# Kernel optimization log

Hardware: AMD Instinct MI355X
Metric: run time of the kernel (lower is better)

## Reference

```python
import jax, jax.numpy as jnp
import numpy as np

B, N, E = 64, 20000, 160000
F_TEXT, HID, OUT = 300, 1024, 1664
NEG_SLOPE = 0.2


def setup_inputs() -> dict:
    key = jax.random.key(0)
    ks = jax.random.split(key, 9)
    img_feat = jax.random.normal(ks[0], (B, OUT), dtype=jnp.float32)
    node_features = jax.random.normal(ks[1], (N, F_TEXT), dtype=jnp.float32)
    edge_src = jax.random.randint(ks[2], (E,), 0, N, dtype=jnp.int32)
    edge_dst = jax.random.randint(ks[3], (E,), 0, N, dtype=jnp.int32)
    edge_weight = jax.random.uniform(ks[4], (E,), dtype=jnp.float32)
    W1 = jax.random.normal(ks[5], (F_TEXT, HID), dtype=jnp.float32) / np.sqrt(F_TEXT)
    b1 = jax.random.normal(ks[6], (HID,), dtype=jnp.float32) * 0.01
    W2 = jax.random.normal(ks[7], (HID, OUT), dtype=jnp.float32) / np.sqrt(HID)
    b2 = jax.random.normal(ks[8], (OUT,), dtype=jnp.float32) * 0.01
    return {"img_feat": img_feat, "node_features": node_features,
            "edge_src": edge_src, "edge_dst": edge_dst, "edge_weight": edge_weight,
            "W1": W1, "b1": b1, "W2": W2, "b2": b2}


def _gcn_norm(edge_src, edge_dst, edge_weight, num_nodes):
    # PyG gcn_norm with add_self_loops=False: symmetric degree normalization
    deg = jax.ops.segment_sum(edge_weight, edge_dst, num_segments=num_nodes)
    dinv = jnp.where(deg > 0, jax.lax.rsqrt(deg), 0.0)
    return dinv[edge_src] * edge_weight * dinv[edge_dst]


def _gcn_conv(x, edge_src, edge_dst, norm, W, b):
    # GCNConv: linear transform, then normalized gather -> scatter-add, then bias
    h = x @ W  # [N, out]
    msgs = h[edge_src] * norm[:, None]  # [E, out] gather + scale
    agg = jax.ops.segment_sum(msgs, edge_dst, num_segments=x.shape[0])
    return agg + b


def reference(img_feat, node_features, edge_src, edge_dst, edge_weight, W1, b1, W2, b2):
    num_nodes = node_features.shape[0]
    norm = _gcn_norm(edge_src, edge_dst, edge_weight, num_nodes)
    x = _gcn_conv(node_features, edge_src, edge_dst, norm, W1, b1)
    x = jnp.where(x >= 0, x, NEG_SLOPE * x)  # leaky_relu(0.2)
    x = _gcn_conv(x, edge_src, edge_dst, norm, W2, b2)
    return img_feat @ x.T  # [B, N]
```

## Files before the change

kernel.cpp:

```cpp
#include <hip/hip_runtime.h>
#include <hip/hip_bf16.h>

#define NNODES 20000
#define NEDGES 160000
#define BQ     64
#define FTEXT  300
#define KPAD1  320
#define HIDDIM 1024
#define OUTDIM 1664

typedef __attribute__((ext_vector_type(8))) short short8;
typedef __attribute__((ext_vector_type(4))) float floatx4;

__device__ inline unsigned short f2bf(float f) {
    union { float f; unsigned int u; } v; v.f = f;
    unsigned int r = v.u + 0x7FFF + ((v.u >> 16) & 1);
    return (unsigned short)(r >> 16);
}
__device__ inline float bf2f(unsigned short h) {
    union { unsigned int u; float f; } v; v.u = ((unsigned int)h) << 16;
    return v.f;
}

__global__ void degcnt_kernel(const int* __restrict__ dst, const float* __restrict__ w,
                              float* __restrict__ deg, int* __restrict__ cnt, int E) {
    int e = blockIdx.x * blockDim.x + threadIdx.x;
    if (e < E) {
        int d = dst[e];
        atomicAdd(&deg[d], w[e]);
        atomicAdd(&cnt[d], 1);
    }
}

__global__ __launch_bounds__(1024) void scan_kernel(const int* __restrict__ cnt,
                                                    int* __restrict__ row_start, int N) {
    __shared__ int partial[1024];
    const int CH = 20;
    int t = threadIdx.x;
    int begin = t * CH;
    int nloc = N - begin; if (nloc > CH) nloc = CH; if (nloc < 0) nloc = 0;
    int vals[CH];
    int s = 0;
    if (nloc == CH) {
        #pragma unroll
        for (int i = 0; i < CH / 4; i++) {
            int4 v = ((const int4*)(cnt + begin))[i];
            vals[i*4+0] = v.x; vals[i*4+1] = v.y; vals[i*4+2] = v.z; vals[i*4+3] = v.w;
            s += v.x + v.y + v.z + v.w;
        }
    } else {
        for (int i = 0; i < nloc; i++) { vals[i] = cnt[begin + i]; s += vals[i]; }
    }
    partial[t] = s;
    __syncthreads();
    for (int off = 1; off < 1024; off <<= 1) {
        int v = (t >= off) ? partial[t - off] : 0;
        __syncthreads();
        partial[t] += v;
        __syncthreads();
    }
    int run = (t == 0) ? 0 : partial[t - 1];
    for (int i = 0; i < nloc; i++) { row_start[begin + i] = run; run += vals[i]; }
    if (t == 1023) row_start[N] = partial[1023];
}

__global__ void fill_kernel(const int* __restrict__ dst, const int* __restrict__ src,
                            const float* __restrict__ w, const float* __restrict__ deg,
                            const int* __restrict__ row_start, int* __restrict__ cursor,
                            int* __restrict__ src_s, float* __restrict__ wnrm_s, int E) {
    int e = blockIdx.x * blockDim.x + threadIdx.x;
    if (e < E) {
        int d = dst[e], s = src[e];
        float dd = deg[d], ds = deg[s];
        float nv = (ds > 0.f ? rsqrtf(ds) : 0.f) * w[e] * (dd > 0.f ? rsqrtf(dd) : 0.f);
        int pos = row_start[d] + atomicAdd(&cursor[d], 1);
        src_s[pos] = s;
        wnrm_s[pos] = nv;
    }
}

__global__ __launch_bounds__(256) void aggnf_kernel(const unsigned short* __restrict__ nfb,
        const int* __restrict__ row_start, const int* __restrict__ src_s,
        const float* __restrict__ wnrm_s, unsigned short* __restrict__ out) {
    int wave = threadIdx.x >> 6, lane = threadIdx.x & 63;
    int d = blockIdx.x * 4 + wave;
    int s0 = row_start[d], s1 = row_start[d + 1];
    float4 acc  = make_float4(0.f, 0.f, 0.f, 0.f);
    float4 acc2 = make_float4(0.f, 0.f, 0.f, 0.f);
    for (int base = s0; base < s1; base += 64) {
        int m = s1 - base; if (m > 64) m = 64;
        int   src_l = (lane < m) ? src_s[base + lane]  : 0;
        float w_l   = (lane < m) ? wnrm_s[base + lane] : 0.f;
        int sj = __shfl(src_l, 0);
        float wj = __shfl(w_l, 0);
        const ushort4* row = (const ushort4*)(nfb + (long)sj * FTEXT);
        ushort4 hv  = row[lane];
        ushort4 hv2 = make_ushort4(0, 0, 0, 0);
        if (lane < 11) hv2 = row[64 + lane];
        for (int j = 0; j < m; j++) {
            ushort4 nv  = make_ushort4(0, 0, 0, 0);
            ushort4 nv2 = make_ushort4(0, 0, 0, 0);
            float wn = 0.f;
            if (j + 1 < m) {
                int sn = __shfl(src_l, j + 1);
                wn = __shfl(w_l, j + 1);
                const ushort4* nrow = (const ushort4*)(nfb + (long)sn * FTEXT);
                nv = nrow[lane];
                if (lane < 11) nv2 = nrow[64 + lane];
            }
            acc.x  += bf2f(hv.x)  * wj; acc.y  += bf2f(hv.y)  * wj;
            acc.z  += bf2f(hv.z)  * wj; acc.w  += bf2f(hv.w)  * wj;
            acc2.x += bf2f(hv2.x) * wj; acc2.y += bf2f(hv2.y) * wj;
            acc2.z += bf2f(hv2.z) * wj; acc2.w += bf2f(hv2.w) * wj;
            hv = nv; hv2 = nv2; wj = wn;
        }
    }
    unsigned short* orow = out + (long)d * KPAD1;
    ushort4 o;
    o.x = f2bf(acc.x); o.y = f2bf(acc.y); o.z = f2bf(acc.z); o.w = f2bf(acc.w);
    ((ushort4*)orow)[lane] = o;
    if (lane < 16) {
        ushort4 o2 = make_ushort4(0, 0, 0, 0);
        if (lane < 11) {
            o2.x = f2bf(acc2.x); o2.y = f2bf(acc2.y);
            o2.z = f2bf(acc2.z); o2.w = f2bf(acc2.w);
        }
        ((ushort4*)orow)[64 + lane] = o2;
    }
}

#define W1N  (HIDDIM * KPAD1)
#define N1F4 (HIDDIM * OUTDIM / 4)
#define N2F4 (BQ * OUTDIM / 4)
#define N3F4 (NNODES * FTEXT / 4)
__global__ void cvt_all_kernel(const float* __restrict__ W1, unsigned short* __restrict__ W1ch,
                               const float* __restrict__ W2, unsigned short* __restrict__ W2b,
                               const float* __restrict__ img, unsigned short* __restrict__ imgb,
                               const float* __restrict__ nf, unsigned short* __restrict__ nfb) {
    int i = blockIdx.x * 256 + threadIdx.x;
    if (i < W1N) {
        int c   = i >> 12;
        int w   = i & 4095;
        int lqg = w >> 10;
        int row = (w >> 3) & 127;
        int j   = i & 7;
        int nt = c / 10, s = c - nt * 10;
        int n = nt * 128 + row;
        int k = s * 32 + lqg * 8 + j;
        float v = (k < FTEXT) ? W1[(long)k * HIDDIM + n] : 0.f;
        W1ch[i] = f2bf(v);
        return;
    }
    i -= W1N;
    const float* in; unsigned short* outp; int j;
    if (i < N1F4)                    { in = W2;  outp = W2b;  j = i; }
    else if (i < N1F4 + N2F4)        { in = img; outp = imgb; j = i - N1F4; }
    else if (i < N1F4 + N2F4 + N3F4) { in = nf;  outp = nfb;  j = i - N1F4 - N2F4; }
    else return;
    float4 v = ((const float4*)in)[j];
    ushort4 o;
    o.x = f2bf(v.x); o.y = f2bf(v.y); o.z = f2bf(v.z); o.w = f2bf(v.w);
    ((ushort4*)outp)[j] = o;
}

__global__ __launch_bounds__(256) void ztcvec_kernel(const float* __restrict__ Ztf,
        unsigned short* __restrict__ Zt, const float* __restrict__ img,
        const float* __restrict__ b2, float* __restrict__ cvec) {
    if (blockIdx.x < (BQ * HIDDIM) / 256) {
        int i = blockIdx.x * 256 + threadIdx.x;
        Zt[i] = f2bf(Ztf[i]);
    } else {
        int b = blockIdx.x - (BQ * HIDDIM) / 256;
        int l = threadIdx.x;
        float v = 0.f;
        for (int f = l; f < OUTDIM; f += 256) v += img[(long)b * OUTDIM + f] * b2[f];
        __shared__ float red[256];
        red[l] = v;
        __syncthreads();
        if (l < 64) {
            v = red[l] + red[l + 64] + red[l + 128] + red[l + 192];
            for (int off = 32; off > 0; off >>= 1) v += __shfl_down(v, off);
            if (l == 0) cvec[b] = v;
        }
    }
}

template<int EPI, int OUT_BF16, int ATOMIC, int NT>
__global__ __launch_bounds__(256) void mfma_gemm(
        const unsigned short* __restrict__ A, const unsigned short* __restrict__ B,
        const float* __restrict__ bias, void* __restrict__ Cv,
        int M, int N, int K, int ldc) {
    constexpr int CT = NT / 16;
    __shared__ unsigned short As[128][40];
    __shared__ unsigned short Bs[NT][40];
    int t = threadIdx.x;
    int m0 = blockIdx.y * 128;
    int n0 = blockIdx.x * NT;
    int klen = K / gridDim.z;
    int kbeg = blockIdx.z * klen;
    int wave = t >> 6, lane = t & 63;
    int lm = lane & 15, lq = lane >> 4;
    floatx4 acc[2][CT] = {};
    for (int k0 = kbeg; k0 < kbeg + klen; k0 += 32) {
        #pragma unroll
        for (int p = 0; p < 2; p++) {
            int idx = p * 256 + t;
            int r = idx >> 2, c8 = (idx & 3) * 8;
            uint4 v = make_uint4(0, 0, 0, 0);
            int gm = m0 + r;
            if (gm < M) v = *(const uint4*)(A + (long)gm * K + k0 + c8);
            *(uint4*)&As[r][c8] = v;
        }
        #pragma unroll
        for (int p = 0; p < NT / 64; p++) {
            int idx = p * 256 + t;
            int r = idx >> 2, c8 = (idx & 3) * 8;
            uint4 v = *(const uint4*)(B + (long)(n0 + r) * K + k0 + c8);
            *(uint4*)&Bs[r][c8] = v;
        }
        __syncthreads();
        short8 a[2], b[CT];
        #pragma unroll
        for (int rt = 0; rt < 2; rt++)
            a[rt] = *(const short8*)&As[wave * 32 + rt * 16 + lm][lq * 8];
        #pragma unroll
        for (int ct = 0; ct < CT; ct++)
            b[ct] = *(const short8*)&Bs[ct * 16 + lm][lq * 8];
        #pragma unroll
        for (int rt = 0; rt < 2; rt++)
            #pragma unroll
            for (int ct = 0; ct < CT; ct++)
                acc[rt][ct] = __builtin_amdgcn_mfma_f32_16x16x32_bf16(
                    a[rt], b[ct], acc[rt][ct], 0, 0, 0);
        __syncthreads();
    }
    #pragma unroll
    for (int rt = 0; rt < 2; rt++) {
        #pragma unroll
        for (int r = 0; r < 4; r++) {
            int gm = m0 + wave * 32 + rt * 16 + lq * 4 + r;
            if (gm >= M) continue;
            #pragma unroll
            for (int ct = 0; ct < CT; ct++) {
                int gn = n0 + ct * 16 + lm;
                float v = acc[rt][ct][r];
                if (EPI) { v += bias[gn]; v = v >= 0.f ? v : 0.2f * v; }
                if (OUT_BF16)      ((unsigned short*)Cv)[(long)gm * ldc + gn] = f2bf(v);
                else if (ATOMIC)   atomicAdd((float*)Cv + (long)gm * ldc + gn, v);
                else               ((float*)Cv)[(long)gm * ldc + gn] = v;
            }
        }
    }
}

__global__ __launch_bounds__(128, 2) void xy_gemm(
        const unsigned short* __restrict__ aggNF, const unsigned short* __restrict__ W1ch,
        const float* __restrict__ b1, const unsigned short* __restrict__ Zt,
        float* __restrict__ Y, int M) {
    __shared__ unsigned short xs[32][136];
    float (*ys)[68] = (float (*)[68])xs;
    int t = threadIdx.x;
    int wn = t >> 6, lane = t & 63;
    int lm = lane & 15, lq = lane >> 4;
    int m0 = blockIdx.x * 32;

    short8 afr[2][10];
    #pragma unroll
    for (int rt = 0; rt < 2; rt++) {
        const unsigned short* ap = aggNF + (long)(m0 + rt * 16 + lm) * KPAD1 + lq * 8;
        #pragma unroll
        for (int kk = 0; kk < 10; kk++)
            afr[rt][kk] = *(const short8*)(ap + kk * 32);
    }
    short8 bcur[4], bnxt[4];
    {
        const unsigned short* bp = W1ch + lq * 1024 + (wn * 64 + lm) * 8;
        #pragma unroll
        for (int ct = 0; ct < 4; ct++) bcur[ct] = *(const short8*)(bp + ct * 128);
    }
    floatx4 yacc[2][4] = {};
    for (int nt = 0; nt < 8; nt++) {
        floatx4 acc[2][4] = {};
        #pragma unroll
        for (int s = 0; s < 10; s++) {
            int c = nt * 10 + s + 1;
            const unsigned short* bp = W1ch + (long)c * 4096 + lq * 1024
                                            + (wn * 64 + lm) * 8;
            #pragma unroll
            for (int ct = 0; ct < 4; ct++) bnxt[ct] = *(const short8*)(bp + ct * 128);
            #pragma unroll
            for (int rt = 0; rt < 2; rt++)
                #pragma unroll
                for (int ct = 0; ct < 4; ct++)
                    acc[rt][ct] = __builtin_amdgcn_mfma_f32_16x16x32_bf16(
                        afr[rt][s], bcur[ct], acc[rt][ct], 0, 0, 0);
            #pragma unroll
            for (int ct = 0; ct < 4; ct++) bcur[ct] = bnxt[ct];
        }
        #pragma unroll
        for (int ct = 0; ct < 4; ct++) {
            int col = wn * 64 + ct * 16 + lm;
            float bv = b1[nt * 128 + col];
            #pragma unroll
            for (int rt = 0; rt < 2; rt++)
                #pragma unroll
                for (int r = 0; r < 4; r++) {
                    float v = acc[rt][ct][r] + bv;
                    v = v >= 0.f ? v : 0.2f * v;
                    xs[rt * 16 + lq * 4 + r][col] = f2bf(v);
                }
        }
        __syncthreads();
        #pragma unroll
        for (int kk2 = 0; kk2 < 2; kk2++) {
            #pragma unroll
            for (int rt = 0; rt < 2; rt++) {
                short8 a = *(const short8*)&xs[rt * 16 + lm][wn * 64 + kk2 * 32 + lq * 8];
                #pragma unroll
                for (int bt = 0; bt < 4; bt++) {
                    short8 b = *(const short8*)(Zt + (long)(bt * 16 + lm) * HIDDIM
                                                    + nt * 128 + wn * 64 + kk2 * 32 + lq * 8);
                    yacc[rt][bt] = __builtin_amdgcn_mfma_f32_16x16x32_bf16(
                        a, b, yacc[rt][bt], 0, 0, 0);
                }
            }
        }
        __syncthreads();
    }
    if (wn == 1) {
        #pragma unroll
        for (int rt = 0; rt < 2; rt++)
            #pragma unroll
            for (int bt = 0; bt < 4; bt++)
                #pragma unroll
                for (int r = 0; r < 4; r++)
                    ys[rt * 16 + lq * 4 + r][bt * 16 + lm] = yacc[rt][bt][r];
    }
    __syncthreads();
    if (wn == 0) {
        #pragma unroll
        for (int rt = 0; rt < 2; rt++)
            #pragma unroll
            for (int bt = 0; bt < 4; bt++)
                #pragma unroll
                for (int r = 0; r < 4; r++) {
                    int row = rt * 16 + lq * 4 + r;
                    Y[(long)(m0 + row) * 64 + bt * 16 + lm]
                        = yacc[rt][bt][r] + ys[row][bt * 16 + lm];
                }
    }
}

__global__ __launch_bounds__(256) void outagg_kernel(const float* __restrict__ Y,
        const int* __restrict__ row_start, const int* __restrict__ src_s,
        const float* __restrict__ wnrm_s, const float* __restrict__ c,
        float* __restrict__ out, int N) {
    __shared__ float tile[4][68];
    int d0 = blockIdx.x * 4;
    int t = threadIdx.x;
    int wave = t >> 6, lane = t & 63;
    int d = d0 + wave;
    int s0 = row_start[d], s1 = row_start[d + 1];
    float acc = 0.f;
    for (int base = s0; base < s1; base += 64) {
        int m = s1 - base; if (m > 64) m = 64;
        int   src_l = (lane < m) ? src_s[base + lane]  : 0;
        float w_l   = (lane < m) ? wnrm_s[base + lane] : 0.f;
        int sj = __shfl(src_l, 0);
        float wj = __shfl(w_l, 0);
        float yv = Y[(long)sj * 64 + lane];
        for (int j = 0; j < m; j++) {
            float yn = 0.f, wn = 0.f;
            if (j + 1 < m) {
                int sn = __shfl(src_l, j + 1);
                wn = __shfl(w_l, j + 1);
                yn = Y[(long)sn * 64 + lane];
            }
            acc += wj * yv;
            yv = yn; wj = wn;
        }
    }
    tile[wave][lane] = acc + c[lane];
    __syncthreads();
    int b = t >> 2, j = t & 3;
    out[(long)b * N + d0 + j] = tile[j][b];
}

extern "C" void kernel_launch(void* const* d_in, const int* in_sizes, int n_in,
                              void* d_out, int out_size, void* d_ws, size_t ws_size,
                              hipStream_t stream) {
    const float* img_feat      = (const float*)d_in[0];
    const float* node_features = (const float*)d_in[1];
    const int*   edge_src      = (const int*)d_in[2];
    const int*   edge_dst      = (const int*)d_in[3];
    const float* edge_weight   = (const float*)d_in[4];
    const float* W1            = (const float*)d_in[5];
    const float* b1            = (const float*)d_in[6];
    const float* W2            = (const float*)d_in[7];
    const float* b2            = (const float*)d_in[8];
    float* out = (float*)d_out;

    const int N = NNODES, E = NEDGES;

    char* ws = (char*)d_ws;
    size_t off = 0;
    auto alloc = [&](size_t bytes) -> void* {
        void* p = ws + off;
        off = (off + bytes + 255) & ~(size_t)255;
        return p;
    };
    float*          deg       = (float*)alloc((size_t)N * 4);
    int*            cnt       = (int*)alloc((size_t)N * 4);
    int*            cursor    = (int*)alloc((size_t)N * 4);
    float*          Ztf       = (float*)alloc((size_t)BQ * HIDDIM * 4);
    size_t zero_bytes = off;
    float*          Y         = (float*)alloc((size_t)N * BQ * 4);
    int*            row_start = (int*)alloc((size_t)(N + 1) * 4);
    int*            src_s     = (int*)alloc((size_t)E * 4);
    float*          wnrm_s    = (float*)alloc((size_t)E * 4);
    unsigned short* aggNF     = (unsigned short*)alloc((size_t)N * KPAD1 * 2);
    unsigned short* W1ch      = (unsigned short*)alloc(((size_t)HIDDIM * KPAD1 + 4096) * 2);
    unsigned short* W2b       = (unsigned short*)alloc((size_t)HIDDIM * OUTDIM * 2);
    unsigned short* imgb      = (unsigned short*)alloc((size_t)BQ * OUTDIM * 2);
    unsigned short* nfb       = (unsigned short*)alloc((size_t)N * FTEXT * 2);
    unsigned short* Zt        = (unsigned short*)alloc((size_t)BQ * HIDDIM * 2);
    float*          cvec      = (float*)alloc((size_t)BQ * 4);

    hipMemsetAsync(ws, 0, zero_bytes, stream);

    int eb = (E + 255) / 256;
    degcnt_kernel<<<eb, 256, 0, stream>>>(edge_dst, edge_weight, deg, cnt, E);
    scan_kernel<<<1, 1024, 0, stream>>>(cnt, row_start, N);
    fill_kernel<<<eb, 256, 0, stream>>>(edge_dst, edge_src, edge_weight, deg, row_start,
                                        cursor, src_s, wnrm_s, E);

    cvt_all_kernel<<<(W1N + (N1F4 + N2F4 + N3F4) + 255) / 256, 256, 0, stream>>>(
        W1, W1ch, W2, W2b, img_feat, imgb, node_features, nfb);

    mfma_gemm<0, 0, 1, 64><<<dim3(HIDDIM / 64, 1, 13), 256, 0, stream>>>(
        imgb, W2b, nullptr, Ztf, BQ, HIDDIM, OUTDIM, HIDDIM);
    ztcvec_kernel<<<(BQ * HIDDIM) / 256 + BQ, 256, 0, stream>>>(Ztf, Zt, img_feat, b2, cvec);

    aggnf_kernel<<<N / 4, 256, 0, stream>>>(nfb, row_start, src_s, wnrm_s, aggNF);

    xy_gemm<<<dim3(NNODES / 32), 128, 0, stream>>>(aggNF, W1ch, b1, Zt, Y, N);

    outagg_kernel<<<N / 4, 256, 0, stream>>>(Y, row_start, src_s, wnrm_s, cvec, out, N);
}
```

Before: 245.8 us.

## Stage W1 panels in LDS via async global_load_lds and split hidden dim across 4 waves

The fused hidden-layer/Y GEMM now loads each 64-column panel of the bf16 W1 into shared memory with direct global-to-LDS loads, instead of every wave streaming W1 fragments from global memory into registers. The block grows to 4 waves, each owning 16 hidden columns per panel and 16 of the 64 output columns of Y, so the final cross-wave reduction through shared memory goes away. W1 is re-laid out in the conversion kernel to match the panel order. The goal is to cut redundant global/L2 traffic for W1 and improve MFMA issue. The cost is a 40KB LDS buffer with extra barriers per panel, and the next panel's load may not fully overlap with compute.

```diff
diff --git a/kernel.cpp b/kernel.cpp
--- a/kernel.cpp
+++ b/kernel.cpp
@@ -20,6 +20,12 @@
 __device__ inline float bf2f(unsigned short h) {
     union { unsigned int u; float f; } v; v.u = ((unsigned int)h) << 16;
     return v.f;
+}
+
+__device__ inline void gload16(const unsigned short* g, unsigned short* l) {
+    __builtin_amdgcn_global_load_lds(
+        (const __attribute__((address_space(1))) unsigned int*)g,
+        (__attribute__((address_space(3))) unsigned int*)l, 16, 0, 0);
 }
 
 __global__ void degcnt_kernel(const int* __restrict__ dst, const float* __restrict__ w,
@@ -139,14 +145,14 @@
                                const float* __restrict__ nf, unsigned short* __restrict__ nfb) {
     int i = blockIdx.x * 256 + threadIdx.x;
     if (i < W1N) {
-        int c   = i >> 12;
-        int w   = i & 4095;
-        int lqg = w >> 10;
-        int row = (w >> 3) & 127;
-        int j   = i & 7;
-        int nt = c / 10, s = c - nt * 10;
-        int n = nt * 128 + row;
-        int k = s * 32 + lqg * 8 + j;
+        int p   = i / 20480;
+        int w   = i - p * 20480;
+        int s   = w >> 11;
+        int lq  = (w >> 9) & 3;
+        int col = (w >> 3) & 63;
+        int j   = w & 7;
+        int n = p * 64 + col;
+        int k = s * 32 + lq * 8 + j;
         float v = (k < FTEXT) ? W1[(long)k * HIDDIM + n] : 0.f;
         W1ch[i] = f2bf(v);
         return;
@@ -253,12 +259,12 @@
     }
 }
 
-__global__ __launch_bounds__(128, 2) void xy_gemm(
+__global__ __launch_bounds__(256, 3) void xy_gemm(
         const unsigned short* __restrict__ aggNF, const unsigned short* __restrict__ W1ch,
         const float* __restrict__ b1, const unsigned short* __restrict__ Zt,
         float* __restrict__ Y, int M) {
-    __shared__ unsigned short xs[32][136];
-    float (*ys)[68] = (float (*)[68])xs;
+    __shared__ unsigned short Bsh[20480];
+    __shared__ unsigned short xs[32][76];
     int t = threadIdx.x;
     int wn = t >> 6, lane = t & 63;
     int lm = lane & 15, lq = lane >> 4;
@@ -272,83 +278,57 @@
         for (int kk = 0; kk < 10; kk++)
             afr[rt][kk] = *(const short8*)(ap + kk * 32);
     }
-    short8 bcur[4], bnxt[4];
     {
-        const unsigned short* bp = W1ch + lq * 1024 + (wn * 64 + lm) * 8;
-        #pragma unroll
-        for (int ct = 0; ct < 4; ct++) bcur[ct] = *(const short8*)(bp + ct * 128);
-    }
-    floatx4 yacc[2][4] = {};
-    for (int nt = 0; nt < 8; nt++) {
-        floatx4 acc[2][4] = {};
+        const unsigned short* src = W1ch + t * 8;
+        #pragma unroll
+        for (int r = 0; r < 10; r++)
+            gload16(src + r * 2048, &Bsh[t * 8 + r * 2048]);
+    }
+    floatx4 yacc[2] = {};
+    for (int p = 0; p < 16; p++) {
+        __syncthreads();
+        floatx4 acc[2] = {};
         #pragma unroll
         for (int s = 0; s < 10; s++) {
-            int c = nt * 10 + s + 1;
-            const unsigned short* bp = W1ch + (long)c * 4096 + lq * 1024
-                                            + (wn * 64 + lm) * 8;
-            #pragma unroll
-            for (int ct = 0; ct < 4; ct++) bnxt[ct] = *(const short8*)(bp + ct * 128);
-            #pragma unroll
-            for (int rt = 0; rt < 2; rt++)
-                #pragma unroll
-                for (int ct = 0; ct < 4; ct++)
-                    acc[rt][ct] = __builtin_amdgcn_mfma_f32_16x16x32_bf16(
-                        afr[rt][s], bcur[ct], acc[rt][ct], 0, 0, 0);
-            #pragma unroll
-            for (int ct = 0; ct < 4; ct++) bcur[ct] = bnxt[ct];
-        }
-        #pragma unroll
-        for (int ct = 0; ct < 4; ct++) {
-            int col = wn * 64 + ct * 16 + lm;
-            float bv = b1[nt * 128 + col];
+            short8 b = *(const short8*)&Bsh[s * 2048 + lq * 512 + (wn * 16 + lm) * 8];
+            acc[0] = __builtin_amdgcn_mfma_f32_16x16x32_bf16(afr[0][s], b, acc[0], 0, 0, 0);
+            acc[1] = __builtin_amdgcn_mfma_f32_16x16x32_bf16(afr[1][s], b, acc[1], 0, 0, 0);
+        }
+        {
+            int col = wn * 16 + lm;
+            float bv = b1[p * 64 + col];
             #pragma unroll
             for (int rt = 0; rt < 2; rt++)
                 #pragma unroll
                 for (int r = 0; r < 4; r++) {
-                    float v = acc[rt][ct][r] + bv;
+                    float v = acc[rt][r] + bv;
                     v = v >= 0.f ? v : 0.2f * v;
                     xs[rt * 16 + lq * 4 + r][col] = f2bf(v);
                 }
         }
         __syncthreads();
-        #pragma unroll
-        for (int kk2 = 0; kk2 < 2; kk2++) {
+        if (p + 1 < 16) {
+            const unsigned short* src = W1ch + (long)(p + 1) * 20480 + t * 8;
+            #pragma unroll
+            for (int r = 0; r < 10; r++)
+                gload16(src + r * 2048, &Bsh[t * 8 + r * 2048]);
+        }
+        #pragma unroll
+        for (int kk = 0; kk < 2; kk++) {
+            short8 b = *(const short8*)(Zt + (long)(wn * 16 + lm) * HIDDIM
+                                            + p * 64 + kk * 32 + lq * 8);
             #pragma unroll
             for (int rt = 0; rt < 2; rt++) {
-                short8 a = *(const short8*)&xs[rt * 16 + lm][wn * 64 + kk2 * 32 + lq * 8];
-                #pragma unroll
-                for (int bt = 0; bt < 4; bt++) {
-                    short8 b = *(const short8*)(Zt + (long)(bt * 16 + lm) * HIDDIM
-                                                    + nt * 128 + wn * 64 + kk2 * 32 + lq * 8);
-                    yacc[rt][bt] = __builtin_amdgcn_mfma_f32_16x16x32_bf16(
-                        a, b, yacc[rt][bt], 0, 0, 0);
-                }
+                short8 a = *(const short8*)&xs[rt * 16 + lm][kk * 32 + lq * 8];
+                yacc[rt] = __builtin_amdgcn_mfma_f32_16x16x32_bf16(a, b, yacc[rt], 0, 0, 0);
             }
         }
-        __syncthreads();
-    }
-    if (wn == 1) {
-        #pragma unroll
-        for (int rt = 0; rt < 2; rt++)
-            #pragma unroll
-            for (int bt = 0; bt < 4; bt++)
-                #pragma unroll
-                for (int r = 0; r < 4; r++)
-                    ys[rt * 16 + lq * 4 + r][bt * 16 + lm] = yacc[rt][bt][r];
-    }
-    __syncthreads();
-    if (wn == 0) {
-        #pragma unroll
-        for (int rt = 0; rt < 2; rt++)
-            #pragma unroll
-            for (int bt = 0; bt < 4; bt++)
-                #pragma unroll
-                for (int r = 0; r < 4; r++) {
-                    int row = rt * 16 + lq * 4 + r;
-                    Y[(long)(m0 + row) * 64 + bt * 16 + lm]
-                        = yacc[rt][bt][r] + ys[row][bt * 16 + lm];
-                }
-    }
+    }
+    #pragma unroll
+    for (int rt = 0; rt < 2; rt++)
+        #pragma unroll
+        for (int r = 0; r < 4; r++)
+            Y[(long)(m0 + rt * 16 + lq * 4 + r) * 64 + wn * 16 + lm] = yacc[rt][r];
 }
 
 __global__ __launch_bounds__(256) void outagg_kernel(const float* __restrict__ Y,
@@ -419,7 +399,7 @@
     int*            src_s     = (int*)alloc((size_t)E * 4);
     float*          wnrm_s    = (float*)alloc((size_t)E * 4);
     unsigned short* aggNF     = (unsigned short*)alloc((size_t)N * KPAD1 * 2);
-    unsigned short* W1ch      = (unsigned short*)alloc(((size_t)HIDDIM * KPAD1 + 4096) * 2);
+    unsigned short* W1ch      = (unsigned short*)alloc((size_t)HIDDIM * KPAD1 * 2);
     unsigned short* W2b       = (unsigned short*)alloc((size_t)HIDDIM * OUTDIM * 2);
     unsigned short* imgb      = (unsigned short*)alloc((size_t)BQ * OUTDIM * 2);
     unsigned short* nfb       = (unsigned short*)alloc((size_t)N * FTEXT * 2);
@@ -443,7 +423,7 @@
 
     aggnf_kernel<<<N / 4, 256, 0, stream>>>(nfb, row_start, src_s, wnrm_s, aggNF);
 
-    xy_gemm<<<dim3(NNODES / 32), 128, 0, stream>>>(aggNF, W1ch, b1, Zt, Y, N);
+    xy_gemm<<<dim3(NNODES / 32), 256, 0, stream>>>(aggNF, W1ch, b1, Zt, Y, N);
 
     outagg_kernel<<<N / 4, 256, 0, stream>>>(Y, row_start, src_s, wnrm_s, cvec, out, N);
 }
```

New measurement: 229.2 us. 1.07x faster.
